# Performance work log

Measured on AMD Instinct MI355X. Metric: run time of the kernel, lower is better.

## Reference

```python
import jax, jax.numpy as jnp
import numpy as np

B, CH, H, W, D = 2, 32, 256, 512, 192


def setup_inputs() -> dict:
    key = jax.random.key(0)
    ks = jax.random.split(key, 10)
    def w(k, shape, fan_in):
        return jax.random.normal(k, shape, jnp.float32) * (1.0 / np.sqrt(fan_in))
    return {
        "x": jax.random.normal(ks[0], (B, CH, H, W), jnp.float32),
        "y": jax.random.normal(ks[1], (B, CH, H, W), jnp.float32),
        # encoder: 1x1 convs ch->64->32->1 (shared for x and y)
        "w1": w(ks[2], (64, CH), CH), "b1": w(ks[3], (64,), CH),
        "w2": w(ks[4], (32, 64), 64), "b2": w(ks[5], (32,), 64),
        "w3": w(ks[6], (1, 32), 32), "b3": w(ks[7], (1,), 32),
        # decoderl: 1x1 conv maxdisp->maxdisp (original code applies decoderl to BOTH volumes)
        "wd": w(ks[8], (D, D), D), "bd": w(ks[9], (D,), D),
    }


def _conv1x1(w, b, h):  # [O,C] x [B,C,H,W] -> [B,O,H,W]
    return jnp.einsum("oc,bchw->bohw", w, h) + b[None, :, None, None]


def _encoder(x, w1, b1, w2, b2, w3, b3):
    h = jax.nn.relu(x)
    h = jax.nn.relu(_conv1x1(w1, b1, h))
    h = jax.nn.relu(_conv1x1(w2, b2, h))
    h = jax.nn.relu(_conv1x1(w3, b3, h))
    return h[:, 0]  # squeeze channel -> [B,H,W]


def _cost_volumes(xf, yf):
    # costx[b,d,h,w] = xf[b,h,w+d] * yf[b,h,w]   (0 where w+d >= W)
    # costy[b,d,h,w] = xf[b,h,w]   * yf[b,h,w-d] (0 where w-d < 0)
    dgrid = jnp.arange(D)
    wgrid = jnp.arange(W)
    x_pad = jnp.pad(xf, ((0, 0), (0, 0), (0, D)))          # zero pad right
    xg = x_pad[:, :, wgrid[None, :] + dgrid[:, None]]       # [B,H,D,W]
    costx = (xg * yf[:, :, None, :]).transpose(0, 2, 1, 3)  # [B,D,H,W]
    y_pad = jnp.pad(yf, ((0, 0), (0, 0), (D, 0)))           # zero pad left
    yg = y_pad[:, :, wgrid[None, :] - dgrid[:, None] + D]   # [B,H,D,W]
    costy = (xf[:, :, None, :] * yg).transpose(0, 2, 1, 3)  # [B,D,H,W]
    return costx, costy


def reference(x, y, w1, b1, w2, b2, w3, b3, wd, bd):
    xf = _encoder(x, w1, b1, w2, b2, w3, b3)
    yf = _encoder(y, w1, b1, w2, b2, w3, b3)
    costx, costy = _cost_volumes(xf, yf)
    probx = jax.nn.softmax(_conv1x1(wd, bd, costx), axis=1)
    proby = jax.nn.softmax(_conv1x1(wd, bd, costy), axis=1)  # decoderl used for both, as in source
    disp_vals = jnp.arange(D, dtype=probx.dtype)
    dispx = jnp.einsum("bdhw,d->bhw", probx, disp_vals)
    dispy = jnp.einsum("bdhw,d->bhw", proby, disp_vals)
    return dispx, dispy
```

## Files before the change

kernel.cpp:

```cpp
#include <hip/hip_runtime.h>


typedef __attribute__((ext_vector_type(8)))  __bf16 bf16x8;
typedef __attribute__((ext_vector_type(8), aligned(4))) __bf16 bf16x8u;
typedef __attribute__((ext_vector_type(4)))  float  f32x4;
typedef __attribute__((ext_vector_type(16))) float  f32x16;

#define MFMA32(a,b,c) __builtin_amdgcn_mfma_f32_32x32x16_bf16((a),(b),(c),0,0,0)
#define MFMA16(a,b,c) __builtin_amdgcn_mfma_f32_16x16x32_bf16((a),(b),(c),0,0,0)

constexpr int WW  = 512;
constexpr int HW  = 256 * 512;
constexpr int CHW = 32 * HW;
constexpr float LOG2E = 1.4426950408889634f;

constexpr size_t XFB_OFF = 0;
constexpr size_t HKG_OFF = 1048576;
constexpr int    HRP     = 2848;
constexpr size_t HDP     = 512ull * HRP;
constexpr size_t WDP_OFF = HKG_OFF + 2 * HDP;
constexpr size_t BDP_OFF = WDP_OFF + 76800;

__global__ __launch_bounds__(512)
void panet_encode(const float* __restrict__ gx,  const float* __restrict__ gy,
                  const float* __restrict__ gw1, const float* __restrict__ gb1,
                  const float* __restrict__ gw2, const float* __restrict__ gb2,
                  const float* __restrict__ gw3, const float* __restrict__ gb3,
                  const float* __restrict__ gwd, const float* __restrict__ gbd,
                  char* __restrict__ ws)
{
  const int blk = blockIdx.x;
  const int tid = threadIdx.x;

  if (blk >= 1024) {
    const int pi = blk - 1024;
    unsigned short* wdp = (unsigned short*)(ws + WDP_OFF);
    for (int idx = tid; idx < 12 * 200; idx += 512) {
      const int oo = idx / 200;
      const int k  = idx - oo * 200;
      const int o  = 12 * pi + oo;
      unsigned short v = 0;
      if (k < 192) v = __builtin_bit_cast(unsigned short, (__bf16)gwd[o * 192 + k]);
      wdp[(o >> 6) * 12800 + (o & 63) * 200 + k] = v;
    }
    unsigned short* hkb = (unsigned short*)(ws + HKG_OFF);
    for (int d = 0; d < 2; ++d)
      for (int rr = 0; rr < 32; ++rr) {
        unsigned short* hk = hkb + d * (HDP / 2) + (size_t)(32 * pi + rr) * (HRP / 2);
        for (int e = 512 + tid; e < 712; e += 512) hk[e] = 0;
        for (int e = 511 + tid; e < 712; e += 512) hk[712 + e] = 0;
      }
    if (pi == 0) {
      float* bdp = (float*)(ws + BDP_OFF);
      if (tid < 192) bdp[tid] = gbd[tid] * LOG2E;
    }
    return;
  }

  const int t    = blk >> 9;
  const int bh   = blk & 511;
  const int lane = tid & 63;
  const int m    = lane & 15;
  const int g    = lane >> 4;
  const int wid  = tid >> 6;

  bf16x8 A1[4], A2[2][2];
  f32x4  bias1[4], bias2[2], w3v[2];
  #pragma unroll
  for (int Mt = 0; Mt < 4; ++Mt) {
    const float* p = gw1 + (16 * Mt + m) * 32 + 4 * g;
    const f32x4 u0 = *(const f32x4*)p;
    const f32x4 u1 = *(const f32x4*)(p + 16);
    #pragma unroll
    for (int j = 0; j < 4; ++j) { A1[Mt][j] = (__bf16)u0[j]; A1[Mt][j + 4] = (__bf16)u1[j]; }
    bias1[Mt] = *(const f32x4*)(gb1 + 16 * Mt + 4 * g);
  }
  #pragma unroll
  for (int Mt = 0; Mt < 2; ++Mt) {
    #pragma unroll
    for (int s = 0; s < 2; ++s) {
      const float* p = gw2 + (16 * Mt + m) * 64 + 32 * s + 4 * g;
      const f32x4 u0 = *(const f32x4*)p;
      const f32x4 u1 = *(const f32x4*)(p + 16);
      #pragma unroll
      for (int j = 0; j < 4; ++j) { A2[Mt][s][j] = (__bf16)u0[j]; A2[Mt][s][j + 4] = (__bf16)u1[j]; }
    }
    bias2[Mt] = *(const f32x4*)(gb2 + 16 * Mt + 4 * g);
    w3v[Mt]   = *(const f32x4*)(gw3 + 16 * Mt + 4 * g);
  }
  const float b3s = gb3[0];
  const f32x4 zf4 = {0.f, 0.f, 0.f, 0.f};
  const float* base = (t ? gy : gx) + (bh >> 8) * CHW + (bh & 255) * WW;
  unsigned short* xfb = (unsigned short*)(ws + XFB_OFF) + t * 262144 + bh * 512;
  unsigned short* hk  = (unsigned short*)(ws + HKG_OFF) + t * (HDP / 2) + (size_t)bh * (HRP / 2);

  for (int u = wid; u < 32; u += 8) {
    const int w0 = u << 4;
    const float* src = base + w0 + m;

    bf16x8 B1;
    #pragma unroll
    for (int j = 0; j < 8; ++j) {
      const int c = 16 * (j >> 2) + 4 * g + (j & 3);
      B1[j] = (__bf16)fmaxf(src[c * HW], 0.f);
    }
    f32x4 acc1[4];
    #pragma unroll
    for (int Mt = 0; Mt < 4; ++Mt) acc1[Mt] = MFMA16(A1[Mt], B1, zf4);

    bf16x8 B2[2];
    #pragma unroll
    for (int s = 0; s < 2; ++s) {
      #pragma unroll
      for (int j = 0; j < 4; ++j) {
        B2[s][j]     = (__bf16)fmaxf(acc1[2 * s][j]     + bias1[2 * s][j],     0.f);
        B2[s][j + 4] = (__bf16)fmaxf(acc1[2 * s + 1][j] + bias1[2 * s + 1][j], 0.f);
      }
    }
    f32x4 acc2[2];
    #pragma unroll
    for (int Mt = 0; Mt < 2; ++Mt)
      acc2[Mt] = MFMA16(A2[Mt][1], B2[1], MFMA16(A2[Mt][0], B2[0], zf4));

    float s3 = 0.f;
    #pragma unroll
    for (int Mt = 0; Mt < 2; ++Mt)
      #pragma unroll
      for (int r = 0; r < 4; ++r)
        s3 += w3v[Mt][r] * fmaxf(acc2[Mt][r] + bias2[Mt][r], 0.f);
    s3 += __shfl_xor(s3, 16);
    s3 += __shfl_xor(s3, 32);
    const float val = fmaxf(s3 + b3s, 0.f);

    if (lane < 16) {
      const int px = w0 + m;
      const unsigned short bits = __builtin_bit_cast(unsigned short, (__bf16)val);
      xfb[px] = bits;
      if (t == 0) {
        hk[px] = bits;
        if (px >= 1) hk[712 + px - 1] = bits;
      } else {
        hk[511 - px] = bits;
        if (px <= 510) hk[712 + 510 - px] = bits;
      }
    }
  }
}

constexpr int K2_BD  = 76800;
constexpr int K2_LDS = 77568;

__global__ __launch_bounds__(256)
void panet_corr(const char* __restrict__ ws, float* __restrict__ gout)
{
  __shared__ __align__(16) char lds[K2_LDS];
  const int tid  = threadIdx.x;

  {
    const f32x4* src = (const f32x4*)(ws + WDP_OFF);
    f32x4* dst = (f32x4*)lds;
    #pragma unroll 4
    for (int i = tid; i < 4800; i += 256) dst[i] = src[i];
    const float* bdp = (const float*)(ws + BDP_OFF);
    if (tid < 192) ((float*)(lds + K2_BD))[tid] = bdp[tid];
  }
  __syncthreads();

  const int lane = tid & 63;
  const int l31  = lane & 31;
  const int h    = lane >> 5;
  const int wid  = tid >> 6;
  const int gw   = blockIdx.x * 4 + wid;
  const int uhalf= gw & 1;
  const int unit = gw >> 1;
  const int dir  = unit >> 9;
  const int bh   = unit & 511;

  const unsigned short* xfbu = (const unsigned short*)(ws + XFB_OFF);
  const unsigned short* ss = xfbu + (dir ? 0 : 262144) + bh * 512;
  const char* hkrow = ws + HKG_OFF + dir * HDP + (size_t)bh * HRP;
  float* outp = gout + dir * 262144 + bh * 512 + uhalf * 256;

  for (int chunk = 0; chunk < 4; ++chunk) {
    const char* bptr[2]; float sc[2];
    #pragma unroll
    for (int ct = 0; ct < 2; ++ct) {
      const int col = uhalf * 256 + chunk * 64 + ct * 32 + l31;
      const int I0  = dir ? (511 - col) : col;
      const int p   = I0 & 1;
      bptr[ct] = hkrow + p * 1424 + 2 * (I0 - p) + 16 * h;
      sc[ct]  = LOG2E * __builtin_bit_cast(float, (unsigned)ss[col] << 16);
    }

    float stS0 = 0.f, stS1 = 0.f, stW0 = 0.f, stW1 = 0.f;

    for (int s = 0; s < 3; ++s) {
      const char* abase = lds + (64 * s + l31) * 400 + 16 * h;
      f32x16 a00 = {0}, a01 = {0}, a10 = {0}, a11 = {0};
      #pragma unroll 3
      for (int ks = 0; ks < 12; ++ks) {
        const bf16x8 af0 = *(const bf16x8*)(abase + 32 * ks);
        const bf16x8 af1 = *(const bf16x8*)(abase + 12800 + 32 * ks);
        const bf16x8 bf0 = __builtin_bit_cast(bf16x8, *(const bf16x8u*)(bptr[0] + 32 * ks));
        const bf16x8 bf1 = __builtin_bit_cast(bf16x8, *(const bf16x8u*)(bptr[1] + 32 * ks));
        a00 = MFMA32(af0, bf0, a00);
        a01 = MFMA32(af0, bf1, a01);
        a10 = MFMA32(af1, bf0, a10);
        a11 = MFMA32(af1, bf1, a11);
      }

      const float obase = (float)(64 * s + 4 * h);
      #pragma unroll
      for (int ct = 0; ct < 2; ++ct) {
        float ls0 = 0.f, ls1 = 0.f, lw0 = 0.f, lw1 = 0.f;
        #pragma unroll
        for (int q = 0; q < 4; ++q) {
          const f32x4 bd0 = *(const f32x4*)(lds + K2_BD + (64 * s + 8 * q + 4 * h) * 4);
          const f32x4 bd1 = *(const f32x4*)(lds + K2_BD + (64 * s + 8 * q + 4 * h + 32) * 4);
          #pragma unroll
          for (int r = 0; r < 4; ++r) {
            const int i = 4 * q + r;
            const float L0 = fmaf(sc[ct], (ct ? a01 : a00)[i], bd0[r]);
            const float L1 = fmaf(sc[ct], (ct ? a11 : a10)[i], bd1[r]);
            const float p0 = __builtin_amdgcn_exp2f(L0);
            const float p1 = __builtin_amdgcn_exp2f(L1);
            const float c  = (float)(r + 8 * q);
            ls0 += p0;  ls1 += p1;
            lw0 = fmaf(c, p0, lw0);
            lw1 = fmaf(c + 32.f, p1, lw1);
          }
        }
        const float ls = ls0 + ls1;
        const float lw = fmaf(obase, ls, lw0 + lw1);
        if (ct == 0) { stS0 += ls; stW0 += lw; }
        else         { stS1 += ls; stW1 += lw; }
      }
    }

    #pragma unroll
    for (int ct = 0; ct < 2; ++ct) {
      float sr = ct ? stS1 : stS0;
      float wr = ct ? stW1 : stW0;
      sr += __shfl_xor(sr, 32);
      wr += __shfl_xor(wr, 32);
      if (lane < 32) outp[chunk * 64 + ct * 32 + l31] = wr / sr;
    }
  }
}

extern "C" void kernel_launch(void* const* d_in, const int* in_sizes, int n_in,
                              void* d_out, int out_size, void* d_ws, size_t ws_size,
                              hipStream_t stream) {
  const float* x  = (const float*)d_in[0];
  const float* y  = (const float*)d_in[1];
  const float* w1 = (const float*)d_in[2];
  const float* b1 = (const float*)d_in[3];
  const float* w2 = (const float*)d_in[4];
  const float* b2 = (const float*)d_in[5];
  const float* w3 = (const float*)d_in[6];
  const float* b3 = (const float*)d_in[7];
  const float* wd = (const float*)d_in[8];
  const float* bd = (const float*)d_in[9];
  char* ws = (char*)d_ws;

  panet_encode<<<1040, 512, 0, stream>>>(x, y, w1, b1, w2, b2, w3, b3, wd, bd, ws);
  panet_corr<<<512, 256, 0, stream>>>(ws, (float*)d_out);
}
```

Before: 98.32 us.

## Build shifted Hankel operand in LDS per row instead of global workspace

The encoder no longer writes duplicated, shifted Hankel copies of the feature rows to global memory. The correlation kernel now runs one 512-thread block per (direction, row) and builds eight shift-aligned copies of the row in LDS, so the MFMA B-operand loads come from aligned LDS instead of unaligned global loads. This removes global write and read traffic and the padding initialisation. In exchange each block re-stages the decoder weights into LDS, and the larger LDS footprint and block size may limit occupancy.

```diff
diff --git a/kernel.cpp b/kernel.cpp
--- a/kernel.cpp
+++ b/kernel.cpp
@@ -2,7 +2,6 @@
 
 
 typedef __attribute__((ext_vector_type(8)))  __bf16 bf16x8;
-typedef __attribute__((ext_vector_type(8), aligned(4))) __bf16 bf16x8u;
 typedef __attribute__((ext_vector_type(4)))  float  f32x4;
 typedef __attribute__((ext_vector_type(16))) float  f32x16;
 
@@ -15,11 +14,9 @@
 constexpr float LOG2E = 1.4426950408889634f;
 
 constexpr size_t XFB_OFF = 0;
-constexpr size_t HKG_OFF = 1048576;
-constexpr int    HRP     = 2848;
-constexpr size_t HDP     = 512ull * HRP;
-constexpr size_t WDP_OFF = HKG_OFF + 2 * HDP;
-constexpr size_t BDP_OFF = WDP_OFF + 76800;
+constexpr int    STB     = 25600;
+constexpr size_t WDP_OFF = 2 * 262144 * 2;
+constexpr size_t BDP_OFF = WDP_OFF + 3 * STB;
 
 __global__ __launch_bounds__(512)
 void panet_encode(const float* __restrict__ gx,  const float* __restrict__ gy,
@@ -43,13 +40,6 @@
       if (k < 192) v = __builtin_bit_cast(unsigned short, (__bf16)gwd[o * 192 + k]);
       wdp[(o >> 6) * 12800 + (o & 63) * 200 + k] = v;
     }
-    unsigned short* hkb = (unsigned short*)(ws + HKG_OFF);
-    for (int d = 0; d < 2; ++d)
-      for (int rr = 0; rr < 32; ++rr) {
-        unsigned short* hk = hkb + d * (HDP / 2) + (size_t)(32 * pi + rr) * (HRP / 2);
-        for (int e = 512 + tid; e < 712; e += 512) hk[e] = 0;
-        for (int e = 511 + tid; e < 712; e += 512) hk[712 + e] = 0;
-      }
     if (pi == 0) {
       float* bdp = (float*)(ws + BDP_OFF);
       if (tid < 192) bdp[tid] = gbd[tid] * LOG2E;
@@ -92,7 +82,6 @@
   const f32x4 zf4 = {0.f, 0.f, 0.f, 0.f};
   const float* base = (t ? gy : gx) + (bh >> 8) * CHW + (bh & 255) * WW;
   unsigned short* xfb = (unsigned short*)(ws + XFB_OFF) + t * 262144 + bh * 512;
-  unsigned short* hk  = (unsigned short*)(ws + HKG_OFF) + t * (HDP / 2) + (size_t)bh * (HRP / 2);
 
   for (int u = wid; u < 32; u += 8) {
     const int w0 = u << 4;
@@ -132,119 +121,120 @@
     s3 += __shfl_xor(s3, 32);
     const float val = fmaxf(s3 + b3s, 0.f);
 
-    if (lane < 16) {
-      const int px = w0 + m;
-      const unsigned short bits = __builtin_bit_cast(unsigned short, (__bf16)val);
-      xfb[px] = bits;
-      if (t == 0) {
-        hk[px] = bits;
-        if (px >= 1) hk[712 + px - 1] = bits;
-      } else {
-        hk[511 - px] = bits;
-        if (px <= 510) hk[712 + 510 - px] = bits;
-      }
-    }
+    if (lane < 16)
+      xfb[w0 + m] = __builtin_bit_cast(unsigned short, (__bf16)val);
   }
 }
 
-constexpr int K2_BD  = 76800;
-constexpr int K2_LDS = 77568;
-
-__global__ __launch_bounds__(256)
+constexpr int CPS    = 1424;
+constexpr int K2_HK  = 76800;
+constexpr int K2_BD  = K2_HK + 8 * CPS;
+constexpr int K2_LDS = K2_BD + 768;
+
+__global__ __launch_bounds__(512)
 void panet_corr(const char* __restrict__ ws, float* __restrict__ gout)
 {
-  __shared__ __align__(16) char lds[K2_LDS];
+  extern __shared__ __align__(16) char lds[];
+  const int blk  = blockIdx.x;
+  const int dir  = blk >> 9;
+  const int bh   = blk & 511;
   const int tid  = threadIdx.x;
-
-  {
-    const f32x4* src = (const f32x4*)(ws + WDP_OFF);
-    f32x4* dst = (f32x4*)lds;
-    #pragma unroll 4
-    for (int i = tid; i < 4800; i += 256) dst[i] = src[i];
-    const float* bdp = (const float*)(ws + BDP_OFF);
-    if (tid < 192) ((float*)(lds + K2_BD))[tid] = bdp[tid];
-  }
-  __syncthreads();
-
   const int lane = tid & 63;
   const int l31  = lane & 31;
   const int h    = lane >> 5;
   const int wid  = tid >> 6;
-  const int gw   = blockIdx.x * 4 + wid;
-  const int uhalf= gw & 1;
-  const int unit = gw >> 1;
-  const int dir  = unit >> 9;
-  const int bh   = unit & 511;
 
   const unsigned short* xfbu = (const unsigned short*)(ws + XFB_OFF);
+  const unsigned short* hs = xfbu + (dir ? 262144 : 0) + bh * 512;
   const unsigned short* ss = xfbu + (dir ? 0 : 262144) + bh * 512;
-  const char* hkrow = ws + HKG_OFF + dir * HDP + (size_t)bh * HRP;
-  float* outp = gout + dir * 262144 + bh * 512 + uhalf * 256;
-
-  for (int chunk = 0; chunk < 4; ++chunk) {
-    const char* bptr[2]; float sc[2];
+
+  {
+    const f32x4* src = (const f32x4*)(ws + WDP_OFF);
+    f32x4* dst = (f32x4*)lds;
+    #pragma unroll 5
+    for (int i = tid; i < 4800; i += 512) dst[i] = src[i];
+    if (tid < 192)
+      ((float*)(lds + K2_BD))[tid] = ((const float*)(ws + BDP_OFF))[tid];
+  }
+  for (int e = tid; e < 712; e += 512) {
+    #pragma unroll
+    for (int c = 0; c < 8; ++c) {
+      const int j = e + c;
+      unsigned short v = 0;
+      if (j <= 511) v = hs[dir ? (511 - j) : j];
+      ((unsigned short*)(lds + K2_HK + c * CPS))[e] = v;
+    }
+  }
+  __syncthreads();
+
+  const char* bptr[2]; float sc[2];
+  #pragma unroll
+  for (int ct = 0; ct < 2; ++ct) {
+    const int col = wid * 64 + ct * 32 + l31;
+    const int I0  = dir ? (511 - col) : col;
+    const int cc  = I0 & 7;
+    bptr[ct] = lds + K2_HK + cc * CPS + 2 * (I0 - cc) + 16 * h;
+    sc[ct]  = LOG2E * __builtin_bit_cast(float, (unsigned)ss[col] << 16);
+  }
+
+  float stS0 = 0.f, stS1 = 0.f, stW0 = 0.f, stW1 = 0.f;
+
+  for (int s = 0; s < 3; ++s) {
+    const char* abase = lds + (64 * s + l31) * 400 + 16 * h;
+    f32x16 a00 = {0}, a01 = {0}, a10 = {0}, a11 = {0};
+    #pragma unroll 4
+    for (int ks = 0; ks < 12; ++ks) {
+      const bf16x8 af0 = *(const bf16x8*)(abase + 32 * ks);
+      const bf16x8 af1 = *(const bf16x8*)(abase + 12800 + 32 * ks);
+      const bf16x8 bf0 = *(const bf16x8*)(bptr[0] + 32 * ks);
+      const bf16x8 bf1 = *(const bf16x8*)(bptr[1] + 32 * ks);
+      a00 = MFMA32(af0, bf0, a00);
+      a01 = MFMA32(af0, bf1, a01);
+      a10 = MFMA32(af1, bf0, a10);
+      a11 = MFMA32(af1, bf1, a11);
+    }
+
+    f32x4 bdr0[4], bdr1[4];
+    #pragma unroll
+    for (int q = 0; q < 4; ++q) {
+      bdr0[q] = *(const f32x4*)(lds + K2_BD + (64 * s + 8 * q + 4 * h) * 4);
+      bdr1[q] = *(const f32x4*)(lds + K2_BD + (64 * s + 8 * q + 4 * h + 32) * 4);
+    }
+    const float obase = (float)(64 * s + 4 * h);
+
     #pragma unroll
     for (int ct = 0; ct < 2; ++ct) {
-      const int col = uhalf * 256 + chunk * 64 + ct * 32 + l31;
-      const int I0  = dir ? (511 - col) : col;
-      const int p   = I0 & 1;
-      bptr[ct] = hkrow + p * 1424 + 2 * (I0 - p) + 16 * h;
-      sc[ct]  = LOG2E * __builtin_bit_cast(float, (unsigned)ss[col] << 16);
-    }
-
-    float stS0 = 0.f, stS1 = 0.f, stW0 = 0.f, stW1 = 0.f;
-
-    for (int s = 0; s < 3; ++s) {
-      const char* abase = lds + (64 * s + l31) * 400 + 16 * h;
-      f32x16 a00 = {0}, a01 = {0}, a10 = {0}, a11 = {0};
-      #pragma unroll 3
-      for (int ks = 0; ks < 12; ++ks) {
-        const bf16x8 af0 = *(const bf16x8*)(abase + 32 * ks);
-        const bf16x8 af1 = *(const bf16x8*)(abase + 12800 + 32 * ks);
-        const bf16x8 bf0 = __builtin_bit_cast(bf16x8, *(const bf16x8u*)(bptr[0] + 32 * ks));
-        const bf16x8 bf1 = __builtin_bit_cast(bf16x8, *(const bf16x8u*)(bptr[1] + 32 * ks));
-        a00 = MFMA32(af0, bf0, a00);
-        a01 = MFMA32(af0, bf1, a01);
-        a10 = MFMA32(af1, bf0, a10);
-        a11 = MFMA32(af1, bf1, a11);
+      float ls0 = 0.f, ls1 = 0.f, lw0 = 0.f, lw1 = 0.f;
+      #pragma unroll
+      for (int q = 0; q < 4; ++q) {
+        #pragma unroll
+        for (int r = 0; r < 4; ++r) {
+          const int i = 4 * q + r;
+          const float L0 = fmaf(sc[ct], (ct ? a01 : a00)[i], bdr0[q][r]);
+          const float L1 = fmaf(sc[ct], (ct ? a11 : a10)[i], bdr1[q][r]);
+          const float p0 = __builtin_amdgcn_exp2f(L0);
+          const float p1 = __builtin_amdgcn_exp2f(L1);
+          const float c  = (float)(r + 8 * q);
+          ls0 += p0;  ls1 += p1;
+          lw0 = fmaf(c, p0, lw0);
+          lw1 = fmaf(c + 32.f, p1, lw1);
+        }
       }
-
-      const float obase = (float)(64 * s + 4 * h);
-      #pragma unroll
-      for (int ct = 0; ct < 2; ++ct) {
-        float ls0 = 0.f, ls1 = 0.f, lw0 = 0.f, lw1 = 0.f;
-        #pragma unroll
-        for (int q = 0; q < 4; ++q) {
-          const f32x4 bd0 = *(const f32x4*)(lds + K2_BD + (64 * s + 8 * q + 4 * h) * 4);
-          const f32x4 bd1 = *(const f32x4*)(lds + K2_BD + (64 * s + 8 * q + 4 * h + 32) * 4);
-          #pragma unroll
-          for (int r = 0; r < 4; ++r) {
-            const int i = 4 * q + r;
-            const float L0 = fmaf(sc[ct], (ct ? a01 : a00)[i], bd0[r]);
-            const float L1 = fmaf(sc[ct], (ct ? a11 : a10)[i], bd1[r]);
-            const float p0 = __builtin_amdgcn_exp2f(L0);
-            const float p1 = __builtin_amdgcn_exp2f(L1);
-            const float c  = (float)(r + 8 * q);
-            ls0 += p0;  ls1 += p1;
-            lw0 = fmaf(c, p0, lw0);
-            lw1 = fmaf(c + 32.f, p1, lw1);
-          }
-        }
-        const float ls = ls0 + ls1;
-        const float lw = fmaf(obase, ls, lw0 + lw1);
-        if (ct == 0) { stS0 += ls; stW0 += lw; }
-        else         { stS1 += ls; stW1 += lw; }
-      }
-    }
-
-    #pragma unroll
-    for (int ct = 0; ct < 2; ++ct) {
-      float sr = ct ? stS1 : stS0;
-      float wr = ct ? stW1 : stW0;
-      sr += __shfl_xor(sr, 32);
-      wr += __shfl_xor(wr, 32);
-      if (lane < 32) outp[chunk * 64 + ct * 32 + l31] = wr / sr;
-    }
+      const float ls = ls0 + ls1;
+      const float lw = fmaf(obase, ls, lw0 + lw1);
+      if (ct == 0) { stS0 += ls; stW0 += lw; }
+      else         { stS1 += ls; stW1 += lw; }
+    }
+  }
+
+  float* outp = gout + dir * 262144 + bh * 512;
+  #pragma unroll
+  for (int ct = 0; ct < 2; ++ct) {
+    float sr = ct ? stS1 : stS0;
+    float wr = ct ? stW1 : stW0;
+    sr += __shfl_xor(sr, 32);
+    wr += __shfl_xor(wr, 32);
+    if (lane < 32) outp[wid * 64 + ct * 32 + l31] = wr / sr;
   }
 }
 
@@ -263,6 +253,8 @@
   const float* bd = (const float*)d_in[9];
   char* ws = (char*)d_ws;
 
+  (void)hipFuncSetAttribute((const void*)panet_corr,
+                            hipFuncAttributeMaxDynamicSharedMemorySize, K2_LDS);
   panet_encode<<<1040, 512, 0, stream>>>(x, y, w1, b1, w2, b2, w3, b3, wd, bd, ws);
-  panet_corr<<<512, 256, 0, stream>>>(ws, (float*)d_out);
+  panet_corr<<<1024, 512, K2_LDS, stream>>>(ws, (float*)d_out);
 }
```

Result: faster. 81.21 us (-17.4%).
